# Optimization experiments

Hardware: AMD Instinct MI355X
Metric: run time of the kernel (lower is better)

## Reference

```python
import jax, jax.numpy as jnp
import numpy as np

B, T, E, H = 8, 1024, 1024, 16
D = E // H  # head_dim = 64
MAX_OFFSET = 0.5


def setup_inputs() -> dict:
    key = jax.random.key(0)
    ks = jax.random.split(key, 12)
    s = 0.02
    return {
        "query": jax.random.normal(ks[0], (B, T, E), jnp.float32),
        "key_": jax.random.normal(ks[1], (B, T, E), jnp.float32),
        "value": jax.random.normal(ks[2], (B, T, E), jnp.float32),
        "Wq": jax.random.normal(ks[3], (E, E), jnp.float32) * s,
        "bq": jnp.zeros((E,), jnp.float32),
        "Wk": jax.random.normal(ks[4], (E, E), jnp.float32) * s,
        "bk": jnp.zeros((E,), jnp.float32),
        "Wv": jax.random.normal(ks[5], (E, E), jnp.float32) * s,
        "bv": jnp.zeros((E,), jnp.float32),
        "Wo": jax.random.normal(ks[6], (E, E), jnp.float32) * s,
        "bo": jnp.zeros((E,), jnp.float32),
        "bias_table": jax.random.normal(ks[7], (2 * T - 1, H), jnp.float32) * s,
        "offset": jax.random.normal(ks[8], (1,), jnp.float32) * 0.1,
    }


def _temporal_bias(bias_table, offset):
    # relative position index: [T, T] in [0, 2T-2]
    coords = jnp.arange(T)
    rel = (coords[:, None] - coords[None, :]) + (T - 1)
    bounded = jnp.tanh(offset) * MAX_OFFSET  # scalar (shape (1,))
    adj = jnp.clip(rel.astype(jnp.float32) + bounded, 0.0, 2.0 * T - 2.0)
    lo = jnp.floor(adj).astype(jnp.int32)
    hi = jnp.ceil(adj).astype(jnp.int32)
    w = adj - lo.astype(jnp.float32)  # [T, T]
    lo_val = bias_table[lo]  # [T, T, H]
    hi_val = bias_table[hi]  # [T, T, H]
    bias = lo_val * (1.0 - w[..., None]) + hi_val * w[..., None]
    # -> [1, H, T, T]
    return jnp.transpose(bias, (2, 0, 1))[None]


def reference(query, key_, value, Wq, bq, Wk, bk, Wv, bv, Wo, bo, bias_table, offset):
    scale = D ** -0.5
    # torch Linear: x @ W.T + b
    q = (jnp.einsum('bte,fe->btf', query, Wq) + bq).reshape(B, T, H, D).transpose(0, 2, 1, 3)
    k = (jnp.einsum('bte,fe->btf', key_, Wk) + bk).reshape(B, T, H, D).transpose(0, 2, 1, 3)
    v = (jnp.einsum('bte,fe->btf', value, Wv) + bv).reshape(B, T, H, D).transpose(0, 2, 1, 3)
    scores = jnp.einsum('bhqd,bhkd->bhqk', q, k) * scale  # [B, H, T, T]
    scores = scores + _temporal_bias(bias_table, offset)
    attn = jax.nn.softmax(scores, axis=-1)
    out = jnp.einsum('bhqk,bhkd->bhqd', attn, v)  # [B, H, T, D]
    out = out.transpose(0, 2, 1, 3).reshape(B, T, E)
    return jnp.einsum('bte,fe->btf', out, Wo) + bo
```

## Files before the change

kernel.cpp:

```cpp
#include <hip/hip_runtime.h>
#include <hip/hip_bf16.h>
#include <stdint.h>

#define B_ 8
#define T_ 1024
#define E_ 1024
#define H_ 16
#define D_ 64
#define NREL 2047

using bf16 = __hip_bfloat16;
typedef __attribute__((ext_vector_type(8))) short bhalf8;
typedef __attribute__((ext_vector_type(4))) float f32x4;

typedef __attribute__((address_space(3))) uint32_t lds32_t;
typedef const __attribute__((address_space(1))) uint32_t glb32_t;
__device__ __forceinline__ void gld_lds16(const bf16* g, bf16* l) {
  __builtin_amdgcn_global_load_lds((glb32_t*)(const void*)g, (lds32_t*)(void*)l, 16, 0, 0);
}

__device__ __forceinline__ bhalf8 cvt8(const float4 a, const float4 b) {
  bf16 t[8];
  t[0] = __float2bfloat16(a.x); t[1] = __float2bfloat16(a.y);
  t[2] = __float2bfloat16(a.z); t[3] = __float2bfloat16(a.w);
  t[4] = __float2bfloat16(b.x); t[5] = __float2bfloat16(b.y);
  t[6] = __float2bfloat16(b.z); t[7] = __float2bfloat16(b.w);
  return *(const bhalf8*)t;
}

__global__ __launch_bounds__(256) void cvt_w4(const float* __restrict__ Wq,
                                              const float* __restrict__ Wk,
                                              const float* __restrict__ Wv,
                                              const float* __restrict__ Wo,
                                              bf16* __restrict__ d) {
  const int z = blockIdx.y;
  const float* s = (z == 0) ? Wq : (z == 1) ? Wk : (z == 2) ? Wv : Wo;
  const int i = (blockIdx.x * 256 + threadIdx.x) * 8;
  const float4 a = *(const float4*)(s + i);
  const float4 b = *(const float4*)(s + i + 4);
  *(bhalf8*)(d + (size_t)z * E_ * E_ + i) = cvt8(a, b);
}

__global__ void bias_pre(const float* __restrict__ table, const float* __restrict__ offset,
                         float* __restrict__ db) {
  const int idx = blockIdx.x * 256 + threadIdx.x;
  if (idx >= NREL * H_) return;
  const int r = idx >> 4;
  const int h = idx & 15;
  const float bounded = tanhf(offset[0]) * 0.5f;
  float adj = (float)r + bounded;
  adj = fminf(fmaxf(adj, 0.f), 2046.f);
  const int lo = (int)floorf(adj);
  const int hi = (int)ceilf(adj);
  const float wgt = adj - (float)lo;
  const float v = table[lo * H_ + h] * (1.f - wgt) + table[hi * H_ + h] * wgt;
  db[h * NREL + r] = v * 1.4426950408889634f;
}

__global__ __launch_bounds__(512, 4) void gemm_qkv(const float* __restrict__ Xq,
                                                   const float* __restrict__ Xk,
                                                   const float* __restrict__ Xv,
                                                   const bf16* __restrict__ Wc,
                                                   const float* __restrict__ bqp,
                                                   const float* __restrict__ bkp,
                                                   const float* __restrict__ bvp,
                                                   bf16* __restrict__ dst) {
  __shared__ bf16 As[2 * 128 * 32];
  __shared__ bf16 Bs[2 * 128 * 32];
  const int tid = threadIdx.x;
  const int lane = tid & 63;
  const int w = tid >> 6;
  const int quad = lane >> 4;
  const int l15 = lane & 15;
  const int m0 = blockIdx.x * 128;
  const int n0 = blockIdx.y * 128;
  const int z = blockIdx.z;
  const float* A = (z == 0) ? Xq : ((z == 1) ? Xk : Xv);
  const float* bias = (z == 0) ? bqp : ((z == 1) ? bkp : bvp);
  const bf16* W = Wc + (size_t)z * E_ * E_;
  bf16* out = dst + (size_t)z * B_ * T_ * D_ * H_;
  const int wm = (w >> 1) * 32;
  const int wn = (w & 1) * 64;

  const f32x4 zero4 = {0.f, 0.f, 0.f, 0.f};
  f32x4 acc[2][4];
#pragma unroll
  for (int i = 0; i < 2; ++i)
#pragma unroll
    for (int j = 0; j < 4; ++j) acc[i][j] = zero4;

  const int srow = w * 16 + (lane >> 2);
  const int scol = (lane & 3) * 8;
  const float* Ag = A + (size_t)(m0 + srow) * E_ + scol;
  const bf16* Wg = W + (size_t)(n0 + srow) * E_ + scol;
  const int sidx = w * 512 + lane * 8;

  float4 p0 = *(const float4*)(Ag);
  float4 p1 = *(const float4*)(Ag + 4);
  *(bhalf8*)(As + sidx) = cvt8(p0, p1);
  gld_lds16(Wg, Bs + sidx);
  p0 = *(const float4*)(Ag + 32);
  p1 = *(const float4*)(Ag + 36);
  __syncthreads();

  for (int kt = 0; kt < 32; ++kt) {
    const int cur = (kt & 1) * 4096;
    bhalf8 af[2], bfr[4];
#pragma unroll
    for (int mt = 0; mt < 2; ++mt)
      af[mt] = *(const bhalf8*)(As + cur + (wm + mt * 16 + l15) * 32 + quad * 8);
#pragma unroll
    for (int nt = 0; nt < 4; ++nt)
      bfr[nt] = *(const bhalf8*)(Bs + cur + (wn + nt * 16 + l15) * 32 + quad * 8);
    if (kt < 31) {
      const int nxt = 4096 - cur;
      const int kc = (kt + 1) * 32;
      gld_lds16(Wg + kc, Bs + nxt + sidx);
      *(bhalf8*)(As + nxt + sidx) = cvt8(p0, p1);
      if (kt < 30) {
        p0 = *(const float4*)(Ag + kc + 32);
        p1 = *(const float4*)(Ag + kc + 36);
      }
    }
#pragma unroll
    for (int mt = 0; mt < 2; ++mt)
#pragma unroll
      for (int nt = 0; nt < 4; ++nt)
        acc[mt][nt] = __builtin_amdgcn_mfma_f32_16x16x32_bf16(af[mt], bfr[nt], acc[mt][nt], 0, 0, 0);
    __syncthreads();
  }

#pragma unroll
  for (int mt = 0; mt < 2; ++mt) {
#pragma unroll
    for (int nt = 0; nt < 4; ++nt) {
      const int n = n0 + wn + nt * 16 + l15;
      const float bv = bias[n];
#pragma unroll
      for (int r = 0; r < 4; ++r) {
        const int m = m0 + wm + mt * 16 + quad * 4 + r;
        const float v = acc[mt][nt][r] + bv;
        const int bb = m >> 10, tq = m & 1023, hh = n >> 6, d = n & 63;
        out[(((size_t)bb * H_ + hh) * T_ + tq) * D_ + d] = __float2bfloat16(v);
      }
    }
  }
}

template <int SCATTER, int F32OUT>
__global__ __launch_bounds__(256) void gemm_bt(const bf16* __restrict__ A,
                                               const bf16* __restrict__ W,
                                               const float* __restrict__ bias,
                                               void* __restrict__ dst_) {
  __shared__ bf16 As[2 * 128 * 32];
  __shared__ bf16 Bs[2 * 128 * 32];
  const int tid = threadIdx.x;
  const int lane = tid & 63;
  const int w = tid >> 6;
  const int quad = lane >> 4;
  const int l15 = lane & 15;
  const int m0 = blockIdx.x * 128;
  const int n0 = blockIdx.y * 128;
  const int wm = (w >> 1) * 64;
  const int wn = (w & 1) * 64;

  const f32x4 zero4 = {0.f, 0.f, 0.f, 0.f};
  f32x4 acc[4][4];
#pragma unroll
  for (int i = 0; i < 4; ++i)
#pragma unroll
    for (int j = 0; j < 4; ++j) acc[i][j] = zero4;

  const int srow0 = w * 32 + (lane >> 2);
  const int scol = (lane & 3) * 8;
  const bf16* Ag = A + (size_t)(m0 + srow0) * E_ + scol;
  const bf16* Wg = W + (size_t)(n0 + srow0) * E_ + scol;
  const int sidx = w * 1024 + lane * 8;

  gld_lds16(Ag, As + sidx);
  gld_lds16(Ag + (size_t)16 * E_, As + sidx + 512);
  gld_lds16(Wg, Bs + sidx);
  gld_lds16(Wg + (size_t)16 * E_, Bs + sidx + 512);
  __syncthreads();

  for (int kt = 0; kt < 32; ++kt) {
    const int cur = (kt & 1) * 4096;
    bhalf8 af[4], bfr[4];
#pragma unroll
    for (int t = 0; t < 4; ++t) {
      af[t] = *(const bhalf8*)(As + cur + (wm + t * 16 + l15) * 32 + quad * 8);
      bfr[t] = *(const bhalf8*)(Bs + cur + (wn + t * 16 + l15) * 32 + quad * 8);
    }
    if (kt < 31) {
      const int nxt = 4096 - cur;
      const int kc = (kt + 1) * 32;
      gld_lds16(Ag + kc, As + nxt + sidx);
      gld_lds16(Ag + (size_t)16 * E_ + kc, As + nxt + sidx + 512);
      gld_lds16(Wg + kc, Bs + nxt + sidx);
      gld_lds16(Wg + (size_t)16 * E_ + kc, Bs + nxt + sidx + 512);
    }
#pragma unroll
    for (int mt = 0; mt < 4; ++mt)
#pragma unroll
      for (int nt = 0; nt < 4; ++nt)
        acc[mt][nt] = __builtin_amdgcn_mfma_f32_16x16x32_bf16(af[mt], bfr[nt], acc[mt][nt], 0, 0, 0);
    __syncthreads();
  }

#pragma unroll
  for (int mt = 0; mt < 4; ++mt) {
#pragma unroll
    for (int nt = 0; nt < 4; ++nt) {
      const int n = n0 + wn + nt * 16 + l15;
      const float bv = bias[n];
#pragma unroll
      for (int r = 0; r < 4; ++r) {
        const int m = m0 + wm + mt * 16 + quad * 4 + r;
        const float v = acc[mt][nt][r] + bv;
        if (SCATTER) {
          const int bb = m >> 10, t = m & 1023, hh = n >> 6, d = n & 63;
          ((bf16*)dst_)[(((size_t)bb * H_ + hh) * T_ + t) * D_ + d] = __float2bfloat16(v);
        } else if (F32OUT) {
          ((float*)dst_)[(size_t)m * E_ + n] = v;
        } else {
          ((bf16*)dst_)[(size_t)m * E_ + n] = __float2bfloat16(v);
        }
      }
    }
  }
}

__device__ __forceinline__ int ps_off(int row, int colbyte) {
  return row * 128 + (colbyte ^ ((row & 7) << 4));
}

__global__ __launch_bounds__(256, 4) void attn_kernel(const bf16* __restrict__ Q,
                                                      const bf16* __restrict__ K,
                                                      const bf16* __restrict__ V,
                                                      const float* __restrict__ db,
                                                      bf16* __restrict__ xout) {
  const int tid = threadIdx.x;
  const int lane = tid & 63;
  const int w = tid >> 6;
  const int quad = lane >> 4;
  const int l15 = lane & 15;
  const int bh = blockIdx.x;
  const int h = bh & 15;
  const int b = bh >> 4;
  const int q0 = blockIdx.y * 128;

  __shared__ bf16 Vt[64][72];
  __shared__ __align__(16) bf16 Ps[4][32 * 64];
  __shared__ float dbs[1152];

  const size_t base = (size_t)bh * T_ * D_;
  const bf16* Qp = Q + base;
  const bf16* Kp = K + base;
  const bf16* Vp = V + base;
  const float* dbh = db + h * NREL;

  for (int t = tid; t < 1151; t += 256) dbs[t] = dbh[q0 + t];

  const int qw = q0 + w * 32;
  bhalf8 aq[2][2];
#pragma unroll
  for (int mt = 0; mt < 2; ++mt)
#pragma unroll
    for (int ks = 0; ks < 2; ++ks)
      aq[mt][ks] = *(const bhalf8*)(Qp + (size_t)(qw + mt * 16 + l15) * D_ + ks * 32 + quad * 8);

  const f32x4 zero4 = {0.f, 0.f, 0.f, 0.f};
  f32x4 o[2][4];
#pragma unroll
  for (int mt = 0; mt < 2; ++mt)
#pragma unroll
    for (int nt = 0; nt < 4; ++nt) o[mt][nt] = zero4;
  float mrow[2] = {-1e30f, -1e30f};
  float lrow[2] = {0.f, 0.f};

  const int vrow0 = tid >> 3;
  const int vc8 = (tid & 7) * 8;
  bhalf8 vreg[2];
  vreg[0] = *(const bhalf8*)(Vp + (size_t)vrow0 * D_ + vc8);
  vreg[1] = *(const bhalf8*)(Vp + (size_t)(vrow0 + 32) * D_ + vc8);

  char* const psw = (char*)&Ps[w][0];

  for (int it = 0; it < 16; ++it) {
    const int kb = it * 64;
    bhalf8 bk[4][2];
#pragma unroll
    for (int nt = 0; nt < 4; ++nt) {
      const bf16* kr = Kp + (size_t)(kb + nt * 16 + l15) * D_ + quad * 8;
      bk[nt][0] = *(const bhalf8*)kr;
      bk[nt][1] = *(const bhalf8*)(kr + 32);
    }

    __syncthreads();
#pragma unroll
    for (int s = 0; s < 2; ++s) {
      const int row = vrow0 + s * 32;
      const bf16* vp = (const bf16*)&vreg[s];
      const int kvp = (row + vc8) & 63;
#pragma unroll
      for (int j = 0; j < 8; ++j) Vt[vc8 + j][kvp] = vp[j];
    }
    __syncthreads();
    if (it < 15) {
      const int kb2 = kb + 64;
      vreg[0] = *(const bhalf8*)(Vp + (size_t)(kb2 + vrow0) * D_ + vc8);
      vreg[1] = *(const bhalf8*)(Vp + (size_t)(kb2 + vrow0 + 32) * D_ + vc8);
    }

    f32x4 s4[2][4];
    __builtin_amdgcn_s_setprio(1);
#pragma unroll
    for (int nt = 0; nt < 4; ++nt) {
#pragma unroll
      for (int mt = 0; mt < 2; ++mt) {
        f32x4 a = zero4;
        a = __builtin_amdgcn_mfma_f32_16x16x32_bf16(bk[nt][0], aq[mt][0], a, 0, 0, 0);
        a = __builtin_amdgcn_mfma_f32_16x16x32_bf16(bk[nt][1], aq[mt][1], a, 0, 0, 0);
        s4[mt][nt] = a;
      }
    }
    __builtin_amdgcn_s_setprio(0);

#pragma unroll
    for (int mt = 0; mt < 2; ++mt) {
      const int ib = w * 32 + mt * 16 + l15 + 1023 - kb;
      float mnt[4];
#pragma unroll
      for (int nt = 0; nt < 4; ++nt) {
#pragma unroll
        for (int r = 0; r < 4; ++r) {
          const float sv = s4[mt][nt][r] * 0.18033688011112042f + dbs[ib - nt * 16 - quad * 4 - r];
          s4[mt][nt][r] = sv;
        }
        mnt[nt] = fmaxf(fmaxf(s4[mt][nt][0], s4[mt][nt][1]),
                        fmaxf(s4[mt][nt][2], s4[mt][nt][3]));
      }
      float tmx = fmaxf(fmaxf(mnt[0], mnt[1]), fmaxf(mnt[2], mnt[3]));
      tmx = fmaxf(tmx, __shfl_xor(tmx, 16, 64));
      tmx = fmaxf(tmx, __shfl_xor(tmx, 32, 64));
      if (!__all(tmx - mrow[mt] <= 11.0f)) {
        const float mnew = fmaxf(mrow[mt], tmx);
        const float alpha = __builtin_amdgcn_exp2f(mrow[mt] - mnew);
        mrow[mt] = mnew;
        lrow[mt] *= alpha;
#pragma unroll
        for (int nt = 0; nt < 4; ++nt) o[mt][nt] *= alpha;
      }
      const float mcur = mrow[mt];
      float psum[4];
#pragma unroll
      for (int nt = 0; nt < 4; ++nt) {
        float p0 = __builtin_amdgcn_exp2f(s4[mt][nt][0] - mcur);
        float p1 = __builtin_amdgcn_exp2f(s4[mt][nt][1] - mcur);
        float p2 = __builtin_amdgcn_exp2f(s4[mt][nt][2] - mcur);
        float p3 = __builtin_amdgcn_exp2f(s4[mt][nt][3] - mcur);
        s4[mt][nt][0] = p0; s4[mt][nt][1] = p1;
        s4[mt][nt][2] = p2; s4[mt][nt][3] = p3;
        psum[nt] = (p0 + p1) + (p2 + p3);
      }
      float sum = (psum[0] + psum[1]) + (psum[2] + psum[3]);
      sum += __shfl_xor(sum, 16, 64);
      sum += __shfl_xor(sum, 32, 64);
      lrow[mt] += sum;

#pragma unroll
      for (int nt = 0; nt < 4; ++nt) {
        alignas(8) bf16 t4[4];
#pragma unroll
        for (int r = 0; r < 4; ++r) t4[r] = __float2bfloat16(s4[mt][nt][r]);
        *(uint2*)(psw + ps_off(mt * 16 + l15, nt * 32 + quad * 8)) = *(const uint2*)t4;
      }
    }

    bhalf8 pb[2][2];
#pragma unroll
    for (int mt = 0; mt < 2; ++mt)
#pragma unroll
      for (int ks = 0; ks < 2; ++ks)
        pb[mt][ks] = *(const bhalf8*)(psw + ps_off(mt * 16 + l15, ks * 64 + quad * 16));
    const int rot = (l15 >> 3);
    __builtin_amdgcn_s_setprio(1);
#pragma unroll
    for (int nt = 0; nt < 4; ++nt) {
      const int drow = nt * 16 + l15;
#pragma unroll
      for (int ks = 0; ks < 2; ++ks) {
        const int gp = (4 * ks + quad + 2 * nt + rot) & 7;
        const bhalf8 vb = *(const bhalf8*)&Vt[drow][gp * 8];
#pragma unroll
        for (int mt = 0; mt < 2; ++mt)
          o[mt][nt] = __builtin_amdgcn_mfma_f32_16x16x32_bf16(vb, pb[mt][ks], o[mt][nt], 0, 0, 0);
      }
    }
    __builtin_amdgcn_s_setprio(0);
  }

#pragma unroll
  for (int mt = 0; mt < 2; ++mt) {
    const float inv = 1.f / lrow[mt];
#pragma unroll
    for (int nt = 0; nt < 4; ++nt) {
      alignas(8) bf16 t4[4];
#pragma unroll
      for (int r = 0; r < 4; ++r) t4[r] = __float2bfloat16(o[mt][nt][r] * inv);
      *(uint2*)(psw + ps_off(mt * 16 + l15, nt * 32 + quad * 8)) = *(const uint2*)t4;
    }
  }
#pragma unroll
  for (int t = 0; t < 4; ++t) {
    const int idx = t * 64 + lane;
    const int row = idx >> 3;
    const int c = idx & 7;
    const bhalf8 val = *(const bhalf8*)(psw + ps_off(row, c * 16));
    *(bhalf8*)&xout[((size_t)b * T_ + qw + row) * E_ + h * D_ + c * 8] = val;
  }
}

extern "C" void kernel_launch(void* const* d_in, const int* in_sizes, int n_in,
                              void* d_out, int out_size, void* d_ws, size_t ws_size,
                              hipStream_t stream) {
  const float* query = (const float*)d_in[0];
  const float* key_  = (const float*)d_in[1];
  const float* value = (const float*)d_in[2];
  const float* Wq = (const float*)d_in[3];
  const float* bq = (const float*)d_in[4];
  const float* Wk = (const float*)d_in[5];
  const float* bk = (const float*)d_in[6];
  const float* Wv = (const float*)d_in[7];
  const float* bv = (const float*)d_in[8];
  const float* Wo = (const float*)d_in[9];
  const float* bo = (const float*)d_in[10];
  const float* table = (const float*)d_in[11];
  const float* offset = (const float*)d_in[12];
  float* out = (float*)d_out;

  char* ws = (char*)d_ws;
  const size_t ME = (size_t)B_ * T_ * E_;
  const size_t EE = (size_t)E_ * E_;
  float* db = (float*)ws;
  bf16* wc  = (bf16*)(ws + 131072);
  bf16* qb  = wc + 4 * EE;
  bf16* kb  = qb + ME;
  bf16* vb2 = kb + ME;
  bf16* x2  = vb2 + ME;

  dim3 bb(256, 1, 1);
  const int gEE = (int)(EE / 8 / 256);

  bias_pre<<<dim3(128), bb, 0, stream>>>(table, offset, db);
  cvt_w4<<<dim3(gEE, 4), bb, 0, stream>>>(Wq, Wk, Wv, Wo, wc);

  gemm_qkv<<<dim3(64, 8, 3), dim3(512), 0, stream>>>(query, key_, value, wc, bq, bk, bv, qb);

  attn_kernel<<<dim3(128, 8, 1), bb, 0, stream>>>(qb, kb, vb2, db, x2);

  gemm_bt<0, 1><<<dim3(64, 8, 1), bb, 0, stream>>>(x2, wc + 3 * EE, bo, out);
}
```

Before: 362.0 us.

## Triple-buffer QKV GEMM weights, retile output GEMM, fuse bias precompute kernel

```diff
diff --git a/kernel.cpp b/kernel.cpp
--- a/kernel.cpp
+++ b/kernel.cpp
@@ -28,12 +28,30 @@
   return *(const bhalf8*)t;
 }
 
-__global__ __launch_bounds__(256) void cvt_w4(const float* __restrict__ Wq,
-                                              const float* __restrict__ Wk,
-                                              const float* __restrict__ Wv,
-                                              const float* __restrict__ Wo,
-                                              bf16* __restrict__ d) {
+__global__ __launch_bounds__(256) void cvt_w4b(const float* __restrict__ Wq,
+                                               const float* __restrict__ Wk,
+                                               const float* __restrict__ Wv,
+                                               const float* __restrict__ Wo,
+                                               bf16* __restrict__ d,
+                                               const float* __restrict__ table,
+                                               const float* __restrict__ offset,
+                                               float* __restrict__ db) {
   const int z = blockIdx.y;
+  if (z == 4) {
+    const int idx = blockIdx.x * 256 + threadIdx.x;
+    if (idx >= NREL * H_) return;
+    const int r = idx >> 4;
+    const int h = idx & 15;
+    const float bounded = tanhf(offset[0]) * 0.5f;
+    float adj = (float)r + bounded;
+    adj = fminf(fmaxf(adj, 0.f), 2046.f);
+    const int lo = (int)floorf(adj);
+    const int hi = (int)ceilf(adj);
+    const float wgt = adj - (float)lo;
+    const float v = table[lo * H_ + h] * (1.f - wgt) + table[hi * H_ + h] * wgt;
+    db[h * NREL + r] = v * 1.4426950408889634f;
+    return;
+  }
   const float* s = (z == 0) ? Wq : (z == 1) ? Wk : (z == 2) ? Wv : Wo;
   const int i = (blockIdx.x * 256 + threadIdx.x) * 8;
   const float4 a = *(const float4*)(s + i);
@@ -41,23 +59,7 @@
   *(bhalf8*)(d + (size_t)z * E_ * E_ + i) = cvt8(a, b);
 }
 
-__global__ void bias_pre(const float* __restrict__ table, const float* __restrict__ offset,
-                         float* __restrict__ db) {
-  const int idx = blockIdx.x * 256 + threadIdx.x;
-  if (idx >= NREL * H_) return;
-  const int r = idx >> 4;
-  const int h = idx & 15;
-  const float bounded = tanhf(offset[0]) * 0.5f;
-  float adj = (float)r + bounded;
-  adj = fminf(fmaxf(adj, 0.f), 2046.f);
-  const int lo = (int)floorf(adj);
-  const int hi = (int)ceilf(adj);
-  const float wgt = adj - (float)lo;
-  const float v = table[lo * H_ + h] * (1.f - wgt) + table[hi * H_ + h] * wgt;
-  db[h * NREL + r] = v * 1.4426950408889634f;
-}
-
-__global__ __launch_bounds__(512, 4) void gemm_qkv(const float* __restrict__ Xq,
+__global__ __launch_bounds__(256, 3) void gemm_qkv(const float* __restrict__ Xq,
                                                    const float* __restrict__ Xk,
                                                    const float* __restrict__ Xv,
                                                    const bf16* __restrict__ Wc,
@@ -66,7 +68,7 @@
                                                    const float* __restrict__ bvp,
                                                    bf16* __restrict__ dst) {
   __shared__ bf16 As[2 * 128 * 32];
-  __shared__ bf16 Bs[2 * 128 * 32];
+  __shared__ bf16 Bs[3 * 128 * 32];
   const int tid = threadIdx.x;
   const int lane = tid & 63;
   const int w = tid >> 6;
@@ -79,59 +81,89 @@
   const float* bias = (z == 0) ? bqp : ((z == 1) ? bkp : bvp);
   const bf16* W = Wc + (size_t)z * E_ * E_;
   bf16* out = dst + (size_t)z * B_ * T_ * D_ * H_;
-  const int wm = (w >> 1) * 32;
+  const int wm = (w >> 1) * 64;
   const int wn = (w & 1) * 64;
 
   const f32x4 zero4 = {0.f, 0.f, 0.f, 0.f};
-  f32x4 acc[2][4];
-#pragma unroll
-  for (int i = 0; i < 2; ++i)
+  f32x4 acc[4][4];
+#pragma unroll
+  for (int i = 0; i < 4; ++i)
 #pragma unroll
     for (int j = 0; j < 4; ++j) acc[i][j] = zero4;
 
-  const int srow = w * 16 + (lane >> 2);
+  const int srow = w * 32 + (lane >> 2);
   const int scol = (lane & 3) * 8;
   const float* Ag = A + (size_t)(m0 + srow) * E_ + scol;
   const bf16* Wg = W + (size_t)(n0 + srow) * E_ + scol;
-  const int sidx = w * 512 + lane * 8;
-
-  float4 p0 = *(const float4*)(Ag);
-  float4 p1 = *(const float4*)(Ag + 4);
-  *(bhalf8*)(As + sidx) = cvt8(p0, p1);
+  const int sidx = w * 1024 + lane * 8;
+
+  {
+    float4 a0 = *(const float4*)(Ag);
+    float4 a1 = *(const float4*)(Ag + 4);
+    float4 a2 = *(const float4*)(Ag + (size_t)16 * E_);
+    float4 a3 = *(const float4*)(Ag + (size_t)16 * E_ + 4);
+    *(bhalf8*)(As + sidx) = cvt8(a0, a1);
+    *(bhalf8*)(As + sidx + 512) = cvt8(a2, a3);
+  }
   gld_lds16(Wg, Bs + sidx);
-  p0 = *(const float4*)(Ag + 32);
-  p1 = *(const float4*)(Ag + 36);
-  __syncthreads();
-
+  gld_lds16(Wg + (size_t)16 * E_, Bs + sidx + 512);
+  gld_lds16(Wg + 32, Bs + 4096 + sidx);
+  gld_lds16(Wg + (size_t)16 * E_ + 32, Bs + 4096 + sidx + 512);
+  float4 p0 = *(const float4*)(Ag + 32);
+  float4 p1 = *(const float4*)(Ag + 36);
+  float4 p2 = *(const float4*)(Ag + (size_t)16 * E_ + 32);
+  float4 p3 = *(const float4*)(Ag + (size_t)16 * E_ + 36);
+  asm volatile("s_waitcnt vmcnt(6)" ::: "memory");
+  asm volatile("s_waitcnt lgkmcnt(0)" ::: "memory");
+  __builtin_amdgcn_s_barrier();
+  __builtin_amdgcn_sched_barrier(0);
+
+  int cB = 0;
+  int cB2 = 2;
   for (int kt = 0; kt < 32; ++kt) {
-    const int cur = (kt & 1) * 4096;
-    bhalf8 af[2], bfr[4];
-#pragma unroll
-    for (int mt = 0; mt < 2; ++mt)
-      af[mt] = *(const bhalf8*)(As + cur + (wm + mt * 16 + l15) * 32 + quad * 8);
-#pragma unroll
-    for (int nt = 0; nt < 4; ++nt)
-      bfr[nt] = *(const bhalf8*)(Bs + cur + (wn + nt * 16 + l15) * 32 + quad * 8);
+    const int curA = (kt & 1) * 4096;
+    bhalf8 af[4], bfr[4];
+#pragma unroll
+    for (int t2 = 0; t2 < 4; ++t2) {
+      af[t2] = *(const bhalf8*)(As + curA + (wm + t2 * 16 + l15) * 32 + quad * 8);
+      bfr[t2] = *(const bhalf8*)(Bs + cB * 4096 + (wn + t2 * 16 + l15) * 32 + quad * 8);
+    }
+    if (kt < 30) {
+      const int kcW = (kt + 2) * 32;
+      gld_lds16(Wg + kcW, Bs + cB2 * 4096 + sidx);
+      gld_lds16(Wg + (size_t)16 * E_ + kcW, Bs + cB2 * 4096 + sidx + 512);
+    }
     if (kt < 31) {
-      const int nxt = 4096 - cur;
-      const int kc = (kt + 1) * 32;
-      gld_lds16(Wg + kc, Bs + nxt + sidx);
-      *(bhalf8*)(As + nxt + sidx) = cvt8(p0, p1);
+      const int nxtA = 4096 - curA;
+      *(bhalf8*)(As + nxtA + sidx) = cvt8(p0, p1);
+      *(bhalf8*)(As + nxtA + sidx + 512) = cvt8(p2, p3);
       if (kt < 30) {
-        p0 = *(const float4*)(Ag + kc + 32);
-        p1 = *(const float4*)(Ag + kc + 36);
-      }
-    }
-#pragma unroll
-    for (int mt = 0; mt < 2; ++mt)
+        const int kc2 = (kt + 2) * 32;
+        p0 = *(const float4*)(Ag + kc2);
+        p1 = *(const float4*)(Ag + kc2 + 4);
+        p2 = *(const float4*)(Ag + (size_t)16 * E_ + kc2);
+        p3 = *(const float4*)(Ag + (size_t)16 * E_ + kc2 + 4);
+      }
+    }
+#pragma unroll
+    for (int mt = 0; mt < 4; ++mt)
 #pragma unroll
       for (int nt = 0; nt < 4; ++nt)
         acc[mt][nt] = __builtin_amdgcn_mfma_f32_16x16x32_bf16(af[mt], bfr[nt], acc[mt][nt], 0, 0, 0);
-    __syncthreads();
-  }
-
-#pragma unroll
-  for (int mt = 0; mt < 2; ++mt) {
+    if (kt < 30) {
+      asm volatile("s_waitcnt vmcnt(6)" ::: "memory");
+      asm volatile("s_waitcnt lgkmcnt(0)" ::: "memory");
+    } else {
+      asm volatile("s_waitcnt vmcnt(0) lgkmcnt(0)" ::: "memory");
+    }
+    __builtin_amdgcn_s_barrier();
+    __builtin_amdgcn_sched_barrier(0);
+    cB = (cB == 2) ? 0 : cB + 1;
+    cB2 = (cB2 == 2) ? 0 : cB2 + 1;
+  }
+
+#pragma unroll
+  for (int mt = 0; mt < 4; ++mt) {
 #pragma unroll
     for (int nt = 0; nt < 4; ++nt) {
       const int n = n0 + wn + nt * 16 + l15;
@@ -148,59 +180,62 @@
 }
 
 template <int SCATTER, int F32OUT>
-__global__ __launch_bounds__(256) void gemm_bt(const bf16* __restrict__ A,
-                                               const bf16* __restrict__ W,
-                                               const float* __restrict__ bias,
-                                               void* __restrict__ dst_) {
-  __shared__ bf16 As[2 * 128 * 32];
+__global__ __launch_bounds__(256, 4) void gemm_bt(const bf16* __restrict__ A,
+                                                  const bf16* __restrict__ W,
+                                                  const float* __restrict__ bias,
+                                                  void* __restrict__ dst_) {
+  __shared__ bf16 As[2 * 64 * 32];
   __shared__ bf16 Bs[2 * 128 * 32];
   const int tid = threadIdx.x;
   const int lane = tid & 63;
   const int w = tid >> 6;
   const int quad = lane >> 4;
   const int l15 = lane & 15;
-  const int m0 = blockIdx.x * 128;
+  const int m0 = blockIdx.x * 64;
   const int n0 = blockIdx.y * 128;
-  const int wm = (w >> 1) * 64;
+  const int wm = (w >> 1) * 32;
   const int wn = (w & 1) * 64;
 
   const f32x4 zero4 = {0.f, 0.f, 0.f, 0.f};
-  f32x4 acc[4][4];
-#pragma unroll
-  for (int i = 0; i < 4; ++i)
+  f32x4 acc[2][4];
+#pragma unroll
+  for (int i = 0; i < 2; ++i)
 #pragma unroll
     for (int j = 0; j < 4; ++j) acc[i][j] = zero4;
 
-  const int srow0 = w * 32 + (lane >> 2);
   const int scol = (lane & 3) * 8;
-  const bf16* Ag = A + (size_t)(m0 + srow0) * E_ + scol;
-  const bf16* Wg = W + (size_t)(n0 + srow0) * E_ + scol;
-  const int sidx = w * 1024 + lane * 8;
-
-  gld_lds16(Ag, As + sidx);
-  gld_lds16(Ag + (size_t)16 * E_, As + sidx + 512);
-  gld_lds16(Wg, Bs + sidx);
-  gld_lds16(Wg + (size_t)16 * E_, Bs + sidx + 512);
+  const int srowA = w * 16 + (lane >> 2);
+  const bf16* Ag = A + (size_t)(m0 + srowA) * E_ + scol;
+  const int sidxA = w * 512 + lane * 8;
+  const int srowB = w * 32 + (lane >> 2);
+  const bf16* Wg = W + (size_t)(n0 + srowB) * E_ + scol;
+  const int sidxB = w * 1024 + lane * 8;
+
+  gld_lds16(Ag, As + sidxA);
+  gld_lds16(Wg, Bs + sidxB);
+  gld_lds16(Wg + (size_t)16 * E_, Bs + sidxB + 512);
   __syncthreads();
 
   for (int kt = 0; kt < 32; ++kt) {
-    const int cur = (kt & 1) * 4096;
-    bhalf8 af[4], bfr[4];
-#pragma unroll
-    for (int t = 0; t < 4; ++t) {
-      af[t] = *(const bhalf8*)(As + cur + (wm + t * 16 + l15) * 32 + quad * 8);
-      bfr[t] = *(const bhalf8*)(Bs + cur + (wn + t * 16 + l15) * 32 + quad * 8);
-    }
+    const int curA = (kt & 1) * 2048;
+    const int curB = (kt & 1) * 4096;
+    bhalf8 af[2], bfr[4];
+#pragma unroll
+    for (int mt = 0; mt < 2; ++mt)
+      af[mt] = *(const bhalf8*)(As + curA + (wm + mt * 16 + l15) * 32 + quad * 8);
+#pragma unroll
+    for (int nt = 0; nt < 4; ++nt)
+      bfr[nt] = *(const bhalf8*)(Bs + curB + (wn + nt * 16 + l15) * 32 + quad * 8);
     if (kt < 31) {
-      const int nxt = 4096 - cur;
+      const int nxtA = 2048 - curA;
+      const int nxtB = 4096 - curB;
       const int kc = (kt + 1) * 32;
-      gld_lds16(Ag + kc, As + nxt + sidx);
-      gld_lds16(Ag + (size_t)16 * E_ + kc, As + nxt + sidx + 512);
-      gld_lds16(Wg + kc, Bs + nxt + sidx);
-      gld_lds16(Wg + (size_t)16 * E_ + kc, Bs + nxt + sidx + 512);
-    }
-#pragma unroll
-    for (int mt = 0; mt < 4; ++mt)
+      gld_lds16(Ag + kc, As + nxtA + sidxA);
+      gld_lds16(Wg + kc, Bs + nxtB + sidxB);
+      gld_lds16(Wg + (size_t)16 * E_ + kc, Bs + nxtB + sidxB + 512);
+    }
+#pragma unroll
+    for (int mt = 0; mt < 2; ++mt)
 #pragma unroll
       for (int nt = 0; nt < 4; ++nt)
         acc[mt][nt] = __builtin_amdgcn_mfma_f32_16x16x32_bf16(af[mt], bfr[nt], acc[mt][nt], 0, 0, 0);
@@ -208,7 +243,7 @@
   }
 
 #pragma unroll
-  for (int mt = 0; mt < 4; ++mt) {
+  for (int mt = 0; mt < 2; ++mt) {
 #pragma unroll
     for (int nt = 0; nt < 4; ++nt) {
       const int n = n0 + wn + nt * 16 + l15;
@@ -452,12 +487,11 @@
   dim3 bb(256, 1, 1);
   const int gEE = (int)(EE / 8 / 256);
 
-  bias_pre<<<dim3(128), bb, 0, stream>>>(table, offset, db);
-  cvt_w4<<<dim3(gEE, 4), bb, 0, stream>>>(Wq, Wk, Wv, Wo, wc);
-
-  gemm_qkv<<<dim3(64, 8, 3), dim3(512), 0, stream>>>(query, key_, value, wc, bq, bk, bv, qb);
+  cvt_w4b<<<dim3(gEE, 5), bb, 0, stream>>>(Wq, Wk, Wv, Wo, wc, table, offset, db);
+
+  gemm_qkv<<<dim3(64, 8, 3), bb, 0, stream>>>(query, key_, value, wc, bq, bk, bv, qb);
 
   attn_kernel<<<dim3(128, 8, 1), bb, 0, stream>>>(qb, kb, vb2, db, x2);
 
-  gemm_bt<0, 1><<<dim3(64, 8, 1), bb, 0, stream>>>(x2, wc + 3 * EE, bo, out);
-}
+  gemm_bt<0, 1><<<dim3(128, 8, 1), bb, 0, stream>>>(x2, wc + 3 * EE, bo, out);
+}
```

New measurement: 350.6 us. 3.2% less time.
